# Kernel tuning notes

Hardware: AMD Instinct MI355X
Metric: run time of the kernel (lower is better)

## Reference

```python
import jax, jax.numpy as jnp
import numpy as np

GRID_SIZE = 30
HIDDEN = 16

def _rbf_kan_layer(x, base_weight, spline_weight, grid):
    # x: [N, in], base_weight: [out, in], spline_weight: [in*G, out]
    base = x @ base_weight.T                                   # [N, out]
    basis = jnp.exp(-20.0 * (x[..., None] - grid) ** 2)        # [N, in, G]
    basis = basis.reshape(x.shape[0], -1)                      # [N, in*G]
    return base + basis @ spline_weight


def setup_inputs() -> dict:
    key = jax.random.key(0)
    ks = jax.random.split(key, 6)
    T = 100000
    t = (jnp.arange(T, dtype=jnp.float32) / T).reshape(T, 1)   # time grid in [0,1), dt = 1/T
    I_init = jax.random.uniform(ks[0], (1,), dtype=jnp.float32) * 0.1
    spline_weight1 = jax.random.normal(ks[1], (1 * GRID_SIZE, HIDDEN), dtype=jnp.float32) * 0.1
    base_weight1 = jax.random.normal(ks[2], (HIDDEN, 1), dtype=jnp.float32) * 0.1
    spline_weight2 = jax.random.normal(ks[3], (HIDDEN * GRID_SIZE, 1), dtype=jnp.float32) * 0.1
    base_weight2 = jax.random.normal(ks[4], (1, HIDDEN), dtype=jnp.float32) * 0.1
    gamma_param = jnp.array([2.0], dtype=jnp.float32)
    return {"t": t, "I_init": I_init,
            "spline_weight1": spline_weight1, "base_weight1": base_weight1,
            "spline_weight2": spline_weight2, "base_weight2": base_weight2,
            "gamma_param": gamma_param}


def reference(t, I_init, spline_weight1, base_weight1, spline_weight2, base_weight2, gamma_param):
    grid = jnp.linspace(0.0, 1.0, GRID_SIZE).astype(t.dtype)
    h = _rbf_kan_layer(t, base_weight1, spline_weight1, grid)      # [T, 16]
    out = _rbf_kan_layer(h, base_weight2, spline_weight2, grid)    # [T, 1]
    betas = jax.nn.softplus(out)                                   # [T, 1]
    gamma = jax.nn.softplus(gamma_param)                           # [1]
    dt = t[1, 0] - t[0, 0]

    I0 = I_init                                                    # [1]
    S0 = 1.0 - I0                                                  # [1]

    def step(carry, beta):
        S, I = carry
        dI = beta * S * I - gamma * I
        S_new = jnp.clip(S - beta * S * I * dt, 0.0, 1.0)
        I_new = jnp.clip(I + dI * dt, 0.0, 1.0)
        return (S_new, I_new), I_new

    _, sim_I = jax.lax.scan(step, (S0, I0), betas)                 # sim_I: [T, 1]
    return sim_I
```

## Files before the change

kernel.cpp:

```cpp
#include <hip/hip_runtime.h>
#include <hip/hip_bf16.h>

#define KAN_GRID 30
#define KAN_HID  16

#define PK   2500
#define PL   40
#define SNPT 10

__global__ __launch_bounds__(256) void kan_betas_kernel(
    const float* __restrict__ t,
    const float* __restrict__ sw1,
    const float* __restrict__ bw1,
    const float* __restrict__ sw2,
    const float* __restrict__ bw2,
    float* __restrict__ beta_dt,
    int T, int K, int L)
{
    __shared__ float s_sw1[KAN_GRID * KAN_HID];
    __shared__ float s_sw2[KAN_HID * KAN_GRID];
    __shared__ float s_bw1[KAN_HID];
    __shared__ float s_bw2[KAN_HID];

    for (int i = threadIdx.x; i < KAN_GRID * KAN_HID; i += blockDim.x) {
        s_sw1[i] = sw1[i];
        s_sw2[i] = sw2[i];
    }
    if (threadIdx.x < KAN_HID) {
        s_bw1[threadIdx.x] = bw1[threadIdx.x];
        s_bw2[threadIdx.x] = bw2[threadIdx.x];
    }
    __syncthreads();

    int m = blockIdx.x * blockDim.x + threadIdx.x;
    if (m >= T) return;

    int n = (m % K) * L + m / K;

    float tv = t[n];
    float dt = t[1] - t[0];

    float h[KAN_HID];
#pragma unroll
    for (int j = 0; j < KAN_HID; ++j) h[j] = tv * s_bw1[j];

#pragma unroll
    for (int g = 0; g < KAN_GRID; ++g) {
        float d = tv - (float)g * (1.0f / 29.0f);
        float e = __expf(-20.0f * d * d);
#pragma unroll
        for (int j = 0; j < KAN_HID; ++j)
            h[j] = fmaf(e, s_sw1[g * KAN_HID + j], h[j]);
    }

    float out = 0.0f;
#pragma unroll
    for (int j = 0; j < KAN_HID; ++j) out = fmaf(h[j], s_bw2[j], out);

#pragma unroll
    for (int j = 0; j < KAN_HID; ++j) {
        float hv = h[j];
#pragma unroll
        for (int g = 0; g < KAN_GRID; ++g) {
            float d = hv - (float)g * (1.0f / 29.0f);
            out = fmaf(__expf(-20.0f * d * d), s_sw2[j * KAN_GRID + g], out);
        }
    }

    float beta = fmaxf(out, 0.0f) + log1pf(__expf(-fabsf(out)));
    beta_dt[m] = beta * dt;
}

#define STEP_O(BDT, DST)                            \
    {                                               \
        float x  = S * I;                           \
        float q  = fmaf(-gdt, I, I);                \
        float Sn = fmaf(-(BDT), x, S);              \
        float In = fmaf((BDT), x, q);               \
        Sn = fminf(fmaxf(Sn, 0.0f), 1.0f);          \
        In = fminf(fmaxf(In, 0.0f), 1.0f);          \
        S = Sn; I = In; (DST) = In;                 \
    }

#define STEP_J(BDT)                                          \
    {                                                        \
        float x  = S * I;                                    \
        float u  = (BDT) * I;                                \
        float v  = (BDT) * S;                                \
        float q  = fmaf(-gdt, I, I);                         \
        float Sn = fmaf(-(BDT), x, S);                       \
        float In = fmaf((BDT), x, q);                        \
        Sn = fminf(fmaxf(Sn, 0.0f), 1.0f);                   \
        In = fminf(fmaxf(In, 0.0f), 1.0f);                   \
        float w  = g1 + v;                                   \
        float a2 = fmaf(-v, jc, fmaf(-u, ja, ja));           \
        float b2 = fmaf(-v, jd, fmaf(-u, jb, jb));           \
        float c2 = fmaf(w, jc, u * ja);                      \
        float d2 = fmaf(w, jd, u * jb);                      \
        S = Sn; I = In; ja = a2; jb = b2; jc = c2; jd = d2;  \
    }

#define SOFTPLUS(X) (fmaxf((X), 0.0f) + log1pf(__expf(-fabsf(X))))

#define COMPOSE(ra,rb,rc,rd,rs,ri, La,Lb,Lc,Ld,Ls,Li, Ea,Eb,Ec,Ed,Es,Ei)   \
    {                                                                      \
        ra = fmaf(La, Ea, Lb * Ec);                                        \
        rb = fmaf(La, Eb, Lb * Ed);                                        \
        rc = fmaf(Lc, Ea, Ld * Ec);                                        \
        rd = fmaf(Lc, Eb, Ld * Ed);                                        \
        rs = fmaf(La, Es, fmaf(Lb, Ei, Ls));                               \
        ri = fmaf(Lc, Es, fmaf(Ld, Ei, Li));                               \
    }

__device__ __forceinline__ void block_affine_scan(
    const float* __restrict__ ja, const float* __restrict__ jb,
    const float* __restrict__ jc, const float* __restrict__ jd,
    const float* __restrict__ cs, const float* __restrict__ ci,
    int K, float S0, float I0,
    float2* g_lds, float (*wm)[6], float (*we)[6])
{
    int tid  = threadIdx.x;
    int lane = tid & 63;
    int wid  = tid >> 6;

    float Fa[SNPT], Fb[SNPT], Fc[SNPT], Fd[SNPT], Fs[SNPT], Fi[SNPT];
    float ma = 1.0f, mb = 0.0f, mc = 0.0f, md = 1.0f, ms = 0.0f, mi = 0.0f;
#pragma unroll
    for (int i = 0; i < SNPT; ++i) {
        int e = tid * SNPT + i;
        if (e < K) {
            Fa[i] = ja[e]; Fb[i] = jb[e]; Fc[i] = jc[e];
            Fd[i] = jd[e]; Fs[i] = cs[e]; Fi[i] = ci[e];
        } else {
            Fa[i] = 1.0f; Fb[i] = 0.0f; Fc[i] = 0.0f;
            Fd[i] = 1.0f; Fs[i] = 0.0f; Fi[i] = 0.0f;
        }
        float na, nb, nc, nd, ns, ni;
        COMPOSE(na,nb,nc,nd,ns,ni, Fa[i],Fb[i],Fc[i],Fd[i],Fs[i],Fi[i],
                                   ma,mb,mc,md,ms,mi);
        ma=na; mb=nb; mc=nc; md=nd; ms=ns; mi=ni;
    }

    for (int off = 1; off < 64; off <<= 1) {
        float pa = __shfl_up(ma, off), pb = __shfl_up(mb, off);
        float pc = __shfl_up(mc, off), pd = __shfl_up(md, off);
        float ps = __shfl_up(ms, off), pi = __shfl_up(mi, off);
        if (lane >= off) {
            float na, nb, nc, nd, ns, ni;
            COMPOSE(na,nb,nc,nd,ns,ni, ma,mb,mc,md,ms,mi, pa,pb,pc,pd,ps,pi);
            ma=na; mb=nb; mc=nc; md=nd; ms=ns; mi=ni;
        }
    }

    if (lane == 63) {
        wm[wid][0]=ma; wm[wid][1]=mb; wm[wid][2]=mc;
        wm[wid][3]=md; wm[wid][4]=ms; wm[wid][5]=mi;
    }
    __syncthreads();

    if (tid == 0) {
        float ra=1.0f, rb=0.0f, rc=0.0f, rd=1.0f, rs=0.0f, ri=0.0f;
        for (int w = 0; w < 4; ++w) {
            we[w][0]=ra; we[w][1]=rb; we[w][2]=rc;
            we[w][3]=rd; we[w][4]=rs; we[w][5]=ri;
            float na, nb, nc, nd, ns, ni;
            COMPOSE(na,nb,nc,nd,ns,ni,
                    wm[w][0],wm[w][1],wm[w][2],wm[w][3],wm[w][4],wm[w][5],
                    ra,rb,rc,rd,rs,ri);
            ra=na; rb=nb; rc=nc; rd=nd; rs=ns; ri=ni;
        }
    }
    __syncthreads();

    float xa = __shfl_up(ma, 1), xb = __shfl_up(mb, 1);
    float xc = __shfl_up(mc, 1), xd = __shfl_up(md, 1);
    float xs = __shfl_up(ms, 1), xi = __shfl_up(mi, 1);
    if (lane == 0) { xa=1.0f; xb=0.0f; xc=0.0f; xd=1.0f; xs=0.0f; xi=0.0f; }
    float Ca, Cb, Cc, Cd, Cs, Ci;
    COMPOSE(Ca,Cb,Cc,Cd,Cs,Ci, xa,xb,xc,xd,xs,xi,
            we[wid][0],we[wid][1],we[wid][2],we[wid][3],we[wid][4],we[wid][5]);

#pragma unroll
    for (int i = 0; i < SNPT; ++i) {
        int e = tid * SNPT + i;
        if (e < K) {
            float gS = fmaf(Ca, S0, fmaf(Cb, I0, Cs));
            float gI = fmaf(Cc, S0, fmaf(Cd, I0, Ci));
            g_lds[e] = make_float2(gS, gI);
        }
        float na, nb, nc, nd, ns, ni;
        COMPOSE(na,nb,nc,nd,ns,ni, Fa[i],Fb[i],Fc[i],Fd[i],Fs[i],Fi[i],
                                   Ca,Cb,Cc,Cd,Cs,Ci);
        Ca=na; Cb=nb; Cc=nc; Cd=nd; Cs=ns; Ci=ni;
    }
    __syncthreads();
}

template<int L>
__global__ __launch_bounds__(256) void sir_chunk_first_kernel(
    const float* __restrict__ t,
    const float* __restrict__ I_init,
    const float* __restrict__ gamma_param,
    const float* __restrict__ beta_t,
    float* __restrict__ o_ja, float* __restrict__ o_jb,
    float* __restrict__ o_jc, float* __restrict__ o_jd,
    float* __restrict__ o_cs, float* __restrict__ o_ci,
    int K)
{
    int k = blockIdx.x * blockDim.x + threadIdx.x;
    if (k >= K) return;

    float dt = t[1] - t[0];
    float gdt = SOFTPLUS(gamma_param[0]) * dt;
    float g1 = 1.0f - gdt;
    float I0 = I_init[0];
    float S0 = 1.0f - I0;

    float S = S0, I = I0;

    float b[L];
#pragma unroll
    for (int s = 0; s < L; ++s) b[s] = beta_t[s * K + k];

    float ja = 1.0f, jb = 0.0f, jc = 0.0f, jd = 1.0f;
#pragma unroll
    for (int s = 0; s < L; ++s) { float bdt = b[s]; STEP_J(bdt); }

    o_ja[k] = ja; o_jb[k] = jb; o_jc[k] = jc; o_jd[k] = jd;
    o_cs[k] = S - fmaf(ja, S0, jb * I0);
    o_ci[k] = I - fmaf(jc, S0, jd * I0);
}

template<int L>
__global__ __launch_bounds__(256) void sir_chunk_scan_kernel(
    const float* __restrict__ t,
    const float* __restrict__ I_init,
    const float* __restrict__ gamma_param,
    const float* __restrict__ beta_t,
    const float* __restrict__ i_ja, const float* __restrict__ i_jb,
    const float* __restrict__ i_jc, const float* __restrict__ i_jd,
    const float* __restrict__ i_cs, const float* __restrict__ i_ci,
    float* __restrict__ o_ja, float* __restrict__ o_jb,
    float* __restrict__ o_jc, float* __restrict__ o_jd,
    float* __restrict__ o_cs, float* __restrict__ o_ci,
    int K)
{
    __shared__ float2 g_lds[PK];
    __shared__ float wm[4][6], we[4][6];

    float dt = t[1] - t[0];
    float gdt = SOFTPLUS(gamma_param[0]) * dt;
    float g1 = 1.0f - gdt;
    float I0 = I_init[0];
    float S0 = 1.0f - I0;

    block_affine_scan(i_ja, i_jb, i_jc, i_jd, i_cs, i_ci,
                      K, S0, I0, g_lds, wm, we);

    int k = blockIdx.x * blockDim.x + threadIdx.x;
    if (k >= K) return;

    float2 g = g_lds[k];
    float S = g.x, I = g.y;

    float b[L];
#pragma unroll
    for (int s = 0; s < L; ++s) b[s] = beta_t[s * K + k];

    float ja = 1.0f, jb = 0.0f, jc = 0.0f, jd = 1.0f;
#pragma unroll
    for (int s = 0; s < L; ++s) { float bdt = b[s]; STEP_J(bdt); }

    o_ja[k] = ja; o_jb[k] = jb; o_jc[k] = jc; o_jd[k] = jd;
    o_cs[k] = S - fmaf(ja, g.x, jb * g.y);
    o_ci[k] = I - fmaf(jc, g.x, jd * g.y);
}

template<int L>
__global__ __launch_bounds__(256) void sir_out_scan_kernel(
    const float* __restrict__ t,
    const float* __restrict__ I_init,
    const float* __restrict__ gamma_param,
    const float* __restrict__ beta_t,
    const float* __restrict__ i_ja, const float* __restrict__ i_jb,
    const float* __restrict__ i_jc, const float* __restrict__ i_jd,
    const float* __restrict__ i_cs, const float* __restrict__ i_ci,
    float* __restrict__ out,
    int K)
{
    __shared__ float2 g_lds[PK];
    __shared__ float wm[4][6], we[4][6];

    float dt = t[1] - t[0];
    float gdt = SOFTPLUS(gamma_param[0]) * dt;
    float I0 = I_init[0];
    float S0 = 1.0f - I0;

    block_affine_scan(i_ja, i_jb, i_jc, i_jd, i_cs, i_ci,
                      K, S0, I0, g_lds, wm, we);

    int k = blockIdx.x * blockDim.x + threadIdx.x;
    if (k >= K) return;

    float2 g = g_lds[k];
    float S = g.x, I = g.y;

    float b[L];
#pragma unroll
    for (int s = 0; s < L; ++s) b[s] = beta_t[s * K + k];

    float r[L];
#pragma unroll
    for (int s = 0; s < L; ++s) { STEP_O(b[s], r[s]); }

    float4* o4 = (float4*)(out + (size_t)k * L);
#pragma unroll
    for (int i = 0; i < L / 4; ++i)
        o4[i] = make_float4(r[4*i], r[4*i+1], r[4*i+2], r[4*i+3]);
}

__global__ void kan_sir_scan_kernel(
    const float* __restrict__ t,
    const float* __restrict__ I_init,
    const float* __restrict__ gamma_param,
    const float* beta_dt,
    float* out,
    int T)
{
    if (threadIdx.x != 0 || blockIdx.x != 0) return;

    float dt = t[1] - t[0];
    float gdt = SOFTPLUS(gamma_param[0]) * dt;

    float I = I_init[0];
    float S = 1.0f - I;

    const float4* b4 = (const float4*)beta_dt;
    float4* o4 = (float4*)out;
    int nvec = T >> 2;

    const int PF = 8;
    float4 buf[PF];
#pragma unroll
    for (int i = 0; i < PF; ++i)
        buf[i] = (i < nvec) ? b4[i] : float4{0.0f, 0.0f, 0.0f, 0.0f};

    for (int base = 0; base < nvec; base += PF) {
#pragma unroll
        for (int i = 0; i < PF; ++i) {
            int c = base + i;
            if (c >= nvec) break;
            float4 b = buf[i];
            int nxt = c + PF;
            if (nxt < nvec) buf[i] = b4[nxt];

            float4 r;
            STEP_O(b.x, r.x);
            STEP_O(b.y, r.y);
            STEP_O(b.z, r.z);
            STEP_O(b.w, r.w);
            o4[c] = r;
        }
    }
    for (int n = nvec << 2; n < T; ++n) {
        float bdt = beta_dt[n];
        float r;
        STEP_O(bdt, r);
        out[n] = r;
    }
}

extern "C" void kernel_launch(void* const* d_in, const int* in_sizes, int n_in,
                              void* d_out, int out_size, void* d_ws, size_t ws_size,
                              hipStream_t stream) {
    const float* t      = (const float*)d_in[0];
    const float* I_init = (const float*)d_in[1];
    const float* sw1    = (const float*)d_in[2];
    const float* bw1    = (const float*)d_in[3];
    const float* sw2    = (const float*)d_in[4];
    const float* bw2    = (const float*)d_in[5];
    const float* gp     = (const float*)d_in[6];
    int T = in_sizes[0];

    float* outf = (float*)d_out;
    float* ws   = (float*)d_ws;
    int bblocks = (T + 255) / 256;

    const int K = PK;
    size_t need = ((size_t)T + 12 * K) * sizeof(float);
    bool fast = (T == PK * PL) && (ws_size >= need);

    if (fast) {
        float* beta_t = ws;
        float* A = ws + T;
        float* B = A + 6 * K;

        kan_betas_kernel<<<bblocks, 256, 0, stream>>>(t, sw1, bw1, sw2, bw2,
                                                      beta_t, T, K, PL);
        int cblocks = (K + 255) / 256;
        sir_chunk_first_kernel<PL><<<cblocks, 256, 0, stream>>>(
            t, I_init, gp, beta_t,
            A, A + K, A + 2*K, A + 3*K, A + 4*K, A + 5*K, K);
        sir_chunk_scan_kernel<PL><<<cblocks, 256, 0, stream>>>(
            t, I_init, gp, beta_t,
            A, A + K, A + 2*K, A + 3*K, A + 4*K, A + 5*K,
            B, B + K, B + 2*K, B + 3*K, B + 4*K, B + 5*K, K);
        sir_out_scan_kernel<PL><<<cblocks, 256, 0, stream>>>(
            t, I_init, gp, beta_t,
            B, B + K, B + 2*K, B + 3*K, B + 4*K, B + 5*K,
            outf, K);
    } else {
        float* betab = (ws_size >= (size_t)T * sizeof(float)) ? ws : outf;
        kan_betas_kernel<<<bblocks, 256, 0, stream>>>(t, sw1, bw1, sw2, bw2,
                                                      betab, T, T, 1);
        kan_sir_scan_kernel<<<1, 64, 0, stream>>>(t, I_init, gp, betab, outf, T);
    }
}
```

Baseline: 41.17 us.

## Fuse three SIR chunk-scan kernels into one cooperative kernel with grid syncs

Merges the chunk-first, chunk-scan and output-scan kernels into a single cooperative kernel launched with 10 blocks. Grid-wide synchronization plus thread fences replace the two kernel-boundary dependencies. The aim is to remove launch overhead and inter-kernel gaps on a small-grid, latency-bound chain. In exchange it adds cooperative-launch overhead and the cost of grid.sync barriers.

After: 65.54 us. 1.59x slower.

```diff
diff --git a/kernel.cpp b/kernel.cpp
--- a/kernel.cpp
+++ b/kernel.cpp
@@ -1,5 +1,8 @@
 #include <hip/hip_runtime.h>
 #include <hip/hip_bf16.h>
+#include <hip/hip_cooperative_groups.h>
+
+namespace cg = cooperative_groups;
 
 #define KAN_GRID 30
 #define KAN_HID  16
@@ -7,6 +10,7 @@
 #define PK   2500
 #define PL   40
 #define SNPT 10
+#define CBLK ((PK + 255) / 256)
 
 __global__ __launch_bounds__(256) void kan_betas_kernel(
     const float* __restrict__ t,
@@ -197,18 +201,20 @@
 }
 
 template<int L>
-__global__ __launch_bounds__(256) void sir_chunk_first_kernel(
+__global__ __launch_bounds__(256) void sir_coop_kernel(
     const float* __restrict__ t,
     const float* __restrict__ I_init,
     const float* __restrict__ gamma_param,
     const float* __restrict__ beta_t,
-    float* __restrict__ o_ja, float* __restrict__ o_jb,
-    float* __restrict__ o_jc, float* __restrict__ o_jd,
-    float* __restrict__ o_cs, float* __restrict__ o_ci,
+    float* __restrict__ A,
+    float* __restrict__ B,
+    float* __restrict__ out,
     int K)
 {
-    int k = blockIdx.x * blockDim.x + threadIdx.x;
-    if (k >= K) return;
+    cg::grid_group grid = cg::this_grid();
+
+    __shared__ float2 g_lds[PK];
+    __shared__ float wm[4][6], we[4][6];
 
     float dt = t[1] - t[0];
     float gdt = SOFTPLUS(gamma_param[0]) * dt;
@@ -216,107 +222,57 @@
     float I0 = I_init[0];
     float S0 = 1.0f - I0;
 
-    float S = S0, I = I0;
-
-    float b[L];
-#pragma unroll
-    for (int s = 0; s < L; ++s) b[s] = beta_t[s * K + k];
-
-    float ja = 1.0f, jb = 0.0f, jc = 0.0f, jd = 1.0f;
-#pragma unroll
-    for (int s = 0; s < L; ++s) { float bdt = b[s]; STEP_J(bdt); }
-
-    o_ja[k] = ja; o_jb[k] = jb; o_jc[k] = jc; o_jd[k] = jd;
-    o_cs[k] = S - fmaf(ja, S0, jb * I0);
-    o_ci[k] = I - fmaf(jc, S0, jd * I0);
-}
-
-template<int L>
-__global__ __launch_bounds__(256) void sir_chunk_scan_kernel(
-    const float* __restrict__ t,
-    const float* __restrict__ I_init,
-    const float* __restrict__ gamma_param,
-    const float* __restrict__ beta_t,
-    const float* __restrict__ i_ja, const float* __restrict__ i_jb,
-    const float* __restrict__ i_jc, const float* __restrict__ i_jd,
-    const float* __restrict__ i_cs, const float* __restrict__ i_ci,
-    float* __restrict__ o_ja, float* __restrict__ o_jb,
-    float* __restrict__ o_jc, float* __restrict__ o_jd,
-    float* __restrict__ o_cs, float* __restrict__ o_ci,
-    int K)
-{
-    __shared__ float2 g_lds[PK];
-    __shared__ float wm[4][6], we[4][6];
-
-    float dt = t[1] - t[0];
-    float gdt = SOFTPLUS(gamma_param[0]) * dt;
-    float g1 = 1.0f - gdt;
-    float I0 = I_init[0];
-    float S0 = 1.0f - I0;
-
-    block_affine_scan(i_ja, i_jb, i_jc, i_jd, i_cs, i_ci,
+    int k = blockIdx.x * blockDim.x + threadIdx.x;
+
+    if (k < K) {
+        float S = S0, I = I0;
+        float b[L];
+#pragma unroll
+        for (int s = 0; s < L; ++s) b[s] = beta_t[s * K + k];
+        float ja = 1.0f, jb = 0.0f, jc = 0.0f, jd = 1.0f;
+#pragma unroll
+        for (int s = 0; s < L; ++s) { float bdt = b[s]; STEP_J(bdt); }
+        A[k]       = ja; A[K + k]   = jb; A[2*K + k] = jc; A[3*K + k] = jd;
+        A[4*K + k] = S - fmaf(ja, S0, jb * I0);
+        A[5*K + k] = I - fmaf(jc, S0, jd * I0);
+    }
+    __threadfence();
+    grid.sync();
+
+    block_affine_scan(A, A + K, A + 2*K, A + 3*K, A + 4*K, A + 5*K,
                       K, S0, I0, g_lds, wm, we);
-
-    int k = blockIdx.x * blockDim.x + threadIdx.x;
-    if (k >= K) return;
-
-    float2 g = g_lds[k];
-    float S = g.x, I = g.y;
-
-    float b[L];
-#pragma unroll
-    for (int s = 0; s < L; ++s) b[s] = beta_t[s * K + k];
-
-    float ja = 1.0f, jb = 0.0f, jc = 0.0f, jd = 1.0f;
-#pragma unroll
-    for (int s = 0; s < L; ++s) { float bdt = b[s]; STEP_J(bdt); }
-
-    o_ja[k] = ja; o_jb[k] = jb; o_jc[k] = jc; o_jd[k] = jd;
-    o_cs[k] = S - fmaf(ja, g.x, jb * g.y);
-    o_ci[k] = I - fmaf(jc, g.x, jd * g.y);
-}
-
-template<int L>
-__global__ __launch_bounds__(256) void sir_out_scan_kernel(
-    const float* __restrict__ t,
-    const float* __restrict__ I_init,
-    const float* __restrict__ gamma_param,
-    const float* __restrict__ beta_t,
-    const float* __restrict__ i_ja, const float* __restrict__ i_jb,
-    const float* __restrict__ i_jc, const float* __restrict__ i_jd,
-    const float* __restrict__ i_cs, const float* __restrict__ i_ci,
-    float* __restrict__ out,
-    int K)
-{
-    __shared__ float2 g_lds[PK];
-    __shared__ float wm[4][6], we[4][6];
-
-    float dt = t[1] - t[0];
-    float gdt = SOFTPLUS(gamma_param[0]) * dt;
-    float I0 = I_init[0];
-    float S0 = 1.0f - I0;
-
-    block_affine_scan(i_ja, i_jb, i_jc, i_jd, i_cs, i_ci,
+    if (k < K) {
+        float2 g = g_lds[k];
+        float S = g.x, I = g.y;
+        float b[L];
+#pragma unroll
+        for (int s = 0; s < L; ++s) b[s] = beta_t[s * K + k];
+        float ja = 1.0f, jb = 0.0f, jc = 0.0f, jd = 1.0f;
+#pragma unroll
+        for (int s = 0; s < L; ++s) { float bdt = b[s]; STEP_J(bdt); }
+        B[k]       = ja; B[K + k]   = jb; B[2*K + k] = jc; B[3*K + k] = jd;
+        B[4*K + k] = S - fmaf(ja, g.x, jb * g.y);
+        B[5*K + k] = I - fmaf(jc, g.x, jd * g.y);
+    }
+    __threadfence();
+    grid.sync();
+
+    block_affine_scan(B, B + K, B + 2*K, B + 3*K, B + 4*K, B + 5*K,
                       K, S0, I0, g_lds, wm, we);
-
-    int k = blockIdx.x * blockDim.x + threadIdx.x;
-    if (k >= K) return;
-
-    float2 g = g_lds[k];
-    float S = g.x, I = g.y;
-
-    float b[L];
-#pragma unroll
-    for (int s = 0; s < L; ++s) b[s] = beta_t[s * K + k];
-
-    float r[L];
-#pragma unroll
-    for (int s = 0; s < L; ++s) { STEP_O(b[s], r[s]); }
-
-    float4* o4 = (float4*)(out + (size_t)k * L);
-#pragma unroll
-    for (int i = 0; i < L / 4; ++i)
-        o4[i] = make_float4(r[4*i], r[4*i+1], r[4*i+2], r[4*i+3]);
+    if (k < K) {
+        float2 g = g_lds[k];
+        float S = g.x, I = g.y;
+        float b[L];
+#pragma unroll
+        for (int s = 0; s < L; ++s) b[s] = beta_t[s * K + k];
+        float r[L];
+#pragma unroll
+        for (int s = 0; s < L; ++s) { STEP_O(b[s], r[s]); }
+        float4* o4 = (float4*)(out + (size_t)k * L);
+#pragma unroll
+        for (int i = 0; i < L / 4; ++i)
+            o4[i] = make_float4(r[4*i], r[4*i+1], r[4*i+2], r[4*i+3]);
+    }
 }
 
 __global__ void kan_sir_scan_kernel(
@@ -397,18 +353,14 @@
 
         kan_betas_kernel<<<bblocks, 256, 0, stream>>>(t, sw1, bw1, sw2, bw2,
                                                       beta_t, T, K, PL);
-        int cblocks = (K + 255) / 256;
-        sir_chunk_first_kernel<PL><<<cblocks, 256, 0, stream>>>(
-            t, I_init, gp, beta_t,
-            A, A + K, A + 2*K, A + 3*K, A + 4*K, A + 5*K, K);
-        sir_chunk_scan_kernel<PL><<<cblocks, 256, 0, stream>>>(
-            t, I_init, gp, beta_t,
-            A, A + K, A + 2*K, A + 3*K, A + 4*K, A + 5*K,
-            B, B + K, B + 2*K, B + 3*K, B + 4*K, B + 5*K, K);
-        sir_out_scan_kernel<PL><<<cblocks, 256, 0, stream>>>(
-            t, I_init, gp, beta_t,
-            B, B + K, B + 2*K, B + 3*K, B + 4*K, B + 5*K,
-            outf, K);
+
+        int Kc = K;
+        void* args[] = { (void*)&t, (void*)&I_init, (void*)&gp, (void*)&beta_t,
+                         (void*)&A, (void*)&B, (void*)&outf, (void*)&Kc };
+        void (*fp)(const float*, const float*, const float*, const float*,
+                   float*, float*, float*, int) = sir_coop_kernel<PL>;
+        hipLaunchCooperativeKernel((void*)fp, dim3(CBLK), dim3(256),
+                                   args, 0, stream);
     } else {
         float* betab = (ws_size >= (size_t)T * sizeof(float)) ? ws : outf;
         kan_betas_kernel<<<bblocks, 256, 0, stream>>>(t, sw1, bw1, sw2, bw2,
```
